# Optimization experiments

Hardware: AMD Instinct MI355X
Metric: run time of the kernel (lower is better)

Reference implementation:

```python
import jax, jax.numpy as jnp
import numpy as np

V = 256   # input_size / vocab
H = 1024  # hidden_size
B = 32
S = 512


def _uniform_w(key, shape, fan_in):
    k = float(np.sqrt(1.0 / fan_in))
    return jax.random.uniform(key, shape, minval=-k, maxval=k, dtype=jnp.float32)


def setup_inputs() -> dict:
    key = jax.random.key(0)
    ks = jax.random.split(key, 8)
    x = jax.random.randint(ks[0], (B, S), 0, V)
    # Gate order along last dim: [i, f, g, o] (concatenated per-gate weights,
    # mathematically identical to 8 separate small matmuls in the original).
    W_x0 = jnp.concatenate([_uniform_w(k, (V, H), V) for k in jax.random.split(ks[1], 4)], axis=1)
    W_h0 = jnp.concatenate([_uniform_w(k, (H, H), H) for k in jax.random.split(ks[2], 4)], axis=1)
    W_x1 = jnp.concatenate([_uniform_w(k, (H, H), H) for k in jax.random.split(ks[3], 4)], axis=1)
    W_h1 = jnp.concatenate([_uniform_w(k, (H, H), H) for k in jax.random.split(ks[4], 4)], axis=1)
    # biases: b_i=0, b_f=1, b_g=0, b_o=0
    b_gate = jnp.concatenate([jnp.zeros(H), jnp.ones(H), jnp.zeros(H), jnp.zeros(H)])
    b0 = b_gate
    b1 = b_gate
    W_hy = _uniform_w(ks[5], (H, V), H)
    b_y = jnp.zeros((V,), dtype=jnp.float32)
    return {"x": x, "W_x0": W_x0, "W_h0": W_h0, "b0": b0,
            "W_x1": W_x1, "W_h1": W_h1, "b1": b1,
            "W_hy": W_hy, "b_y": b_y}


def _cell(gates, c_prev):
    i, f, g, o = jnp.split(gates, 4, axis=-1)
    c = jax.nn.sigmoid(f) * c_prev + jax.nn.sigmoid(i) * jnp.tanh(g)
    h = jax.nn.sigmoid(o) * jnp.tanh(c)
    return h, c


def reference(x, W_x0, W_h0, b0, W_x1, W_h1, b1, W_hy, b_y):
    # x: (B, S) int -> one-hot (S, B, V)
    xe = jax.nn.one_hot(x, V, dtype=W_x0.dtype)          # (B, S, V)
    # precompute layer-0 input projection for all timesteps (same math)
    xproj = jnp.einsum('bsv,vg->sbg', xe, W_x0) + b0     # (S, B, 4H)

    def step(carry, xp_t):
        h0, c0, h1, c1 = carry
        h0n, c0n = _cell(xp_t + h0 @ W_h0, c0)
        h1n, c1n = _cell(h0n @ W_x1 + h1 @ W_h1 + b1, c1)
        out = h1n @ W_hy + b_y                           # (B, V)
        return (h0n, c0n, h1n, c1n), out

    z = jnp.zeros((x.shape[0], H), dtype=W_x0.dtype)
    _, outs = jax.lax.scan(step, (z, z, z, z), xproj)
    return outs                                          # (S, B, V)
```

## Files before the change

kernel.cpp:

```cpp
#include <hip/hip_runtime.h>
#include <math.h>


typedef __attribute__((ext_vector_type(8))) short short8;
typedef __attribute__((ext_vector_type(4))) float f32x4;

constexpr int kV = 256, kH = 1024, kB = 32, kS = 512, G4H = 4096;
constexpr int NT = 512, NBLK = 208;
constexpr int NA = 64, B0 = 64, C0 = 192, ROOT = NBLK - 1;

constexpr long SZW = 4194304L;
constexpr long SZY = 262144L;
constexpr long WP0H = 0,        WP0L = SZW;
constexpr long WP1XH = 2*SZW,   WP1XL = 3*SZW;
constexpr long WP1HH = 4*SZW,   WP1HL = 5*SZW;
constexpr long WYH  = 6*SZW,    WYL  = 6*SZW + SZY;
constexpr long HOFF = 6*SZW + 2*SZY;

#define MFMA(a,b,c) __builtin_amdgcn_mfma_f32_16x16x32_bf16(a, b, c, 0, 0, 0)

#define VM_WAIT(n) do { \
    asm volatile("s_waitcnt vmcnt(" #n ")" ::: "memory"); \
    __builtin_amdgcn_sched_barrier(0); \
  } while (0)

#define WLOAD(dst, p) \
  asm volatile("global_load_dwordx4 %0, %1, off" : "=v"(dst) : "v"(p) : "memory")

__device__ __forceinline__ float sigmoidf_(float v) { return 1.f / (1.f + expf(-v)); }

__device__ __forceinline__ void bf16split(float w, unsigned& hi, unsigned& lo) {
  unsigned u = __float_as_uint(w);
  unsigned r = (u + 0x7fffu + ((u >> 16) & 1u)) >> 16;
  float res = w - __uint_as_float(r << 16);
  unsigned u2 = __float_as_uint(res);
  unsigned r2 = (u2 + 0x7fffu + ((u2 >> 16) & 1u)) >> 16;
  hi = r; lo = r2;
}


__device__ __forceinline__ void coh_store_u32(unsigned* p, unsigned v) {
  asm volatile("global_store_dword %0, %1, off sc0 sc1" :: "v"(p), "v"(v) : "memory");
}
__device__ __forceinline__ void coh_store_u16(unsigned short* p, unsigned v) {
  asm volatile("global_store_short %0, %1, off sc0 sc1" :: "v"(p), "v"(v) : "memory");
}
__device__ __forceinline__ unsigned coh_load_u32(const unsigned* p) {
  unsigned v;
  asm volatile("global_load_dword %0, %1, off sc0 sc1\n\ts_waitcnt vmcnt(0)"
               : "=v"(v) : "v"(p) : "memory");
  return v;
}

__device__ __forceinline__ void stage_issue4(const unsigned short* pr0h,
                                             const unsigned short* pr1h,
                                             const unsigned short* pr0l,
                                             const unsigned short* pr1l,
                                             int qoff,
                                             float4& a, float4& b,
                                             float4& c, float4& d) {
  asm volatile(
      "global_load_dwordx4 %0, %4, off sc0 sc1\n\t"
      "global_load_dwordx4 %1, %5, off sc0 sc1\n\t"
      "global_load_dwordx4 %2, %6, off sc0 sc1\n\t"
      "global_load_dwordx4 %3, %7, off sc0 sc1"
      : "=&v"(a), "=&v"(b), "=&v"(c), "=&v"(d)
      : "v"(pr0h + qoff), "v"(pr1h + qoff), "v"(pr0l + qoff), "v"(pr1l + qoff)
      : "memory");
}

__device__ __forceinline__ void stage_write4(short8* HH, short8* HL,
                                             int b0_, int kg,
                                             const float4& a, const float4& b,
                                             const float4& c, const float4& d) {
  HH[b0_ * 33 + kg]        = __builtin_bit_cast(short8, a);
  HH[(b0_ + 16) * 33 + kg] = __builtin_bit_cast(short8, b);
  HL[b0_ * 33 + kg]        = __builtin_bit_cast(short8, c);
  HL[(b0_ + 16) * 33 + kg] = __builtin_bit_cast(short8, d);
}

__device__ __forceinline__ void lds_barrier() {
  asm volatile("s_waitcnt lgkmcnt(0)" ::: "memory");
  __builtin_amdgcn_sched_barrier(0);
  __builtin_amdgcn_s_barrier();
  __builtin_amdgcn_sched_barrier(0);
}


__device__ __forceinline__ void flag_barrier(unsigned* arrive, unsigned* gen,
                                             int blk, int tid, int t) {
  __syncthreads();
  const unsigned target = (unsigned)(t + 1);
  if (tid == 0) coh_store_u32(arrive + blk * 16, target);
  if (blk == ROOT) {
    if (tid < 64) {
      const unsigned* q0 = arrive + tid * 16;
      const unsigned* q1 = arrive + (64 + tid) * 16;
      const unsigned* q2 = arrive + (128 + tid) * 16;
      const int i3 = (192 + tid < NBLK) ? (192 + tid) : 0;
      const unsigned* q3 = arrive + i3 * 16;
      int guard = 0;
      for (;;) {
        unsigned a, b, c, d;
        asm volatile(
            "global_load_dword %0, %4, off sc0 sc1\n\t"
            "global_load_dword %1, %5, off sc0 sc1\n\t"
            "global_load_dword %2, %6, off sc0 sc1\n\t"
            "global_load_dword %3, %7, off sc0 sc1\n\t"
            "s_waitcnt vmcnt(0)"
            : "=&v"(a), "=&v"(b), "=&v"(c), "=&v"(d)
            : "v"(q0), "v"(q1), "v"(q2), "v"(q3) : "memory");
        bool ok = (a >= target) && (b >= target) && (c >= target) && (d >= target);
        if (__all(ok)) break;
        if (++guard > (1 << 17)) break;
      }
      if (tid == 0) coh_store_u32(gen, target);
    }
  } else {
    if (tid == 0) {
      int guard = 0;
      while (coh_load_u32(gen) < target) {
        __builtin_amdgcn_s_sleep(1);
        if (++guard > (1 << 17)) break;
      }
    }
  }
  __syncthreads();
}


__global__ void pack_w(const float* __restrict__ in, unsigned short* __restrict__ hi,
                       unsigned short* __restrict__ lo, int ncols) {
  int id = blockIdx.x * 256 + threadIdx.x;
  int slab = id / ncols, row = id % ncols;
  int k0 = (slab >> 2) * 32 + (slab & 3) * 8;
  long ob = ((long)slab * ncols + row) * 8;
  #pragma unroll
  for (int e = 0; e < 8; ++e) {
    float w = in[(long)(k0 + e) * ncols + row];
    unsigned h_, l_;
    bf16split(w, h_, l_);
    hi[ob + e] = (unsigned short)h_;
    lo[ob + e] = (unsigned short)l_;
  }
}

__global__ void zero_state(unsigned* __restrict__ p, int n) {
  int i = blockIdx.x * 256 + threadIdx.x;
  if (i < n) p[i] = 0u;
}


extern "C" __global__ void __launch_bounds__(512, 1)
lstm_persist(const int* __restrict__ x,
             const float* __restrict__ Wx0,
             const float* __restrict__ b0v,
             const float* __restrict__ b1v,
             const float* __restrict__ byv,
             unsigned short* __restrict__ wss,
             float* __restrict__ out) {
  const short8* wp0h  = (const short8*)(wss + WP0H);
  const short8* wp0l  = (const short8*)(wss + WP0L);
  const short8* wp1xh = (const short8*)(wss + WP1XH);
  const short8* wp1xl = (const short8*)(wss + WP1XL);
  const short8* wp1hh = (const short8*)(wss + WP1HH);
  const short8* wp1hl = (const short8*)(wss + WP1HL);
  const short8* wyh   = (const short8*)(wss + WYH);
  const short8* wyl   = (const short8*)(wss + WYL);
  unsigned short* h0h = wss + HOFF;
  unsigned short* h0l = h0h + 65536;
  unsigned short* h1h = h0h + 131072;
  unsigned short* h1l = h0h + 196608;
  unsigned* arrive = (unsigned*)(h0h + 262144);
  unsigned* gen = arrive + 4096;

  const int tid = threadIdx.x, blk = blockIdx.x;
  const int lane = tid & 63, m = lane & 15, quad = lane >> 4, w = tid >> 6;
  const int b0_ = tid >> 5, kg = tid & 31;
  const int kg8 = kg * 8;

  __shared__ short8 HSH[2][32 * 33];
  __shared__ short8 HSL[2][32 * 33];
  __shared__ float gx[4096];

  if (blk < NA) {
    const int g = w >> 1, kh = w & 1, j0A = blk * 16;
    const int ue = tid >> 5, be = tid & 31, j2e = j0A + ue;
    const float bA0 = b0v[j2e],          bA1 = b0v[kH + j2e];
    const float bA2 = b0v[2 * kH + j2e], bA3 = b0v[3 * kH + j2e];
    const short8* ah_ = wp0h + quad * 4096 + (g * 1024 + j0A + m);
    const short8* al_ = wp0l + quad * 4096 + (g * 1024 + j0A + m);
    short8 wah[16], wal[16];
    #pragma unroll
    for (int i = 0; i < 16; ++i) {
      WLOAD(wah[i], &ah_[(2 * i + kh) * 16384]);
      WLOAD(wal[i], &al_[(2 * i + kh) * 16384]);
    }
    VM_WAIT(0);
    float c0r = 0.f;

    #pragma unroll 1
    for (int t = 0; t < kS + 2; ++t) {
      const int s = t;
      if (s < kS) {
        const int rpar = (s + 1) & 1;
        const unsigned short* gH = h0h + rpar * 32768;
        const unsigned short* gL = h0l + rpar * 32768;
        const unsigned short* pH0 = gH + b0_ * 1024 + kg8;
        const unsigned short* pH1 = pH0 + 16 * 1024;
        const unsigned short* pL0 = gL + b0_ * 1024 + kg8;
        const unsigned short* pL1 = pL0 + 16 * 1024;
        const int xs = x[be * kS + s];
        const float* wxp = Wx0 + (long)xs * G4H + j2e;
        float wxi, wxf, wxg, wxo;
        asm volatile(
            "global_load_dword %0, %4, off\n\t"
            "global_load_dword %1, %5, off\n\t"
            "global_load_dword %2, %6, off\n\t"
            "global_load_dword %3, %7, off"
            : "=&v"(wxi), "=&v"(wxf), "=&v"(wxg), "=&v"(wxo)
            : "v"(wxp), "v"(wxp + kH), "v"(wxp + 2 * kH), "v"(wxp + 3 * kH)
            : "memory");
        float4 st[2][4];
        stage_issue4(pH0, pH1, pL0, pL1, 0, st[0][0], st[0][1], st[0][2], st[0][3]);
        f32x4 acc0 = {0.f, 0.f, 0.f, 0.f}, acc1 = {0.f, 0.f, 0.f, 0.f};
        #pragma unroll
        for (int ph = 0; ph < 4; ++ph) {
          if (ph < 3)
            stage_issue4(pH0, pH1, pL0, pL1, (ph + 1) * 256,
                         st[(ph + 1) & 1][0], st[(ph + 1) & 1][1],
                         st[(ph + 1) & 1][2], st[(ph + 1) & 1][3]);
          if (ph < 3) { VM_WAIT(4); } else { VM_WAIT(0); }
          stage_write4(&HSH[ph & 1][0], &HSL[ph & 1][0], b0_, kg,
                       st[ph & 1][0], st[ph & 1][1], st[ph & 1][2], st[ph & 1][3]);
          lds_barrier();
          #pragma unroll
          for (int i2 = 0; i2 < 4; ++i2) {
            const int kl = 2 * i2 + kh;
            const int widx = ph * 4 + i2;
            short8 bh0 = HSH[ph & 1][m * 33 + kl * 4 + quad];
            short8 bl0 = HSL[ph & 1][m * 33 + kl * 4 + quad];
            short8 bh1 = HSH[ph & 1][(16 + m) * 33 + kl * 4 + quad];
            short8 bl1 = HSL[ph & 1][(16 + m) * 33 + kl * 4 + quad];
            acc0 = MFMA(wah[widx], bh0, acc0);
            acc0 = MFMA(wah[widx], bl0, acc0);
            acc0 = MFMA(wal[widx], bh0, acc0);
            acc1 = MFMA(wah[widx], bh1, acc1);
            acc1 = MFMA(wah[widx], bl1, acc1);
            acc1 = MFMA(wal[widx], bh1, acc1);
          }
        }
        #pragma unroll
        for (int r = 0; r < 4; ++r) {
          gx[(kh * 64 + g * 16 + quad * 4 + r) * 32 + m]      = acc0[r];
          gx[(kh * 64 + g * 16 + quad * 4 + r) * 32 + 16 + m] = acc1[r];
        }
        lds_barrier();
        {
          float gi = gx[(0 + ue) * 32 + be]  + gx[(64 + 0 + ue) * 32 + be]  + wxi + bA0;
          float gf = gx[(16 + ue) * 32 + be] + gx[(64 + 16 + ue) * 32 + be] + wxf + bA1;
          float gg = gx[(32 + ue) * 32 + be] + gx[(64 + 32 + ue) * 32 + be] + wxg + bA2;
          float go = gx[(48 + ue) * 32 + be] + gx[(64 + 48 + ue) * 32 + be] + wxo + bA3;
          float cc = sigmoidf_(gf) * c0r + sigmoidf_(gi) * tanhf(gg);
          float hh = sigmoidf_(go) * tanhf(cc);
          c0r = cc;
          unsigned h_, l_;
          bf16split(hh, h_, l_);
          const int wpar = s & 1;
          coh_store_u16(h0h + wpar * 32768 + be * 1024 + j2e, h_);
          coh_store_u16(h0l + wpar * 32768 + be * 1024 + j2e, l_);
        }
      }
      if (t < kS + 1) flag_barrier(arrive, gen, blk, tid, t);
    }
  } else if (blk < C0) {
    const int hf = w >> 2, mt = (w >> 1) & 1, kq = w & 1;
    const int rowB = mt * 16 + m;
    const int growB = (rowB >> 3) * 1024 + (blk - B0) * 8 + (rowB & 7);
    const int ub = tid >> 5, bb2 = tid & 31;
    const int j2b = (blk - B0) * 8 + (ub & 7);
    const float bB0 = b1v[j2b],          bB1 = b1v[kH + j2b];
    const float bB2 = b1v[2 * kH + j2b], bB3 = b1v[3 * kH + j2b];
    const short8* bh_ = (hf ? wp1hh : wp1xh) + quad * 4096 + growB;
    const short8* bl_ = (hf ? wp1hl : wp1xl) + quad * 4096 + growB;
    short8 wbh[16], wbl[16];
    #pragma unroll
    for (int i = 0; i < 16; ++i) {
      WLOAD(wbh[i], &bh_[(2 * i + kq) * 16384]);
      WLOAD(wbl[i], &bl_[(2 * i + kq) * 16384]);
    }
    VM_WAIT(0);
    float c1r = 0.f;

    #pragma unroll 1
    for (int t = 0; t < kS + 2; ++t) {
      const int s = t - 1;
      if (s >= 0 && s < kS) {
        const unsigned short* g0h = h0h + (s & 1) * 32768;
        const unsigned short* g0l = h0l + (s & 1) * 32768;
        const unsigned short* g1h = h1h + ((s + 1) & 1) * 32768;
        const unsigned short* g1l = h1l + ((s + 1) & 1) * 32768;
        const unsigned short* pA0h = g0h + b0_ * 1024 + kg8;
        const unsigned short* pA1h = pA0h + 16 * 1024;
        const unsigned short* pA0l = g0l + b0_ * 1024 + kg8;
        const unsigned short* pA1l = pA0l + 16 * 1024;
        const unsigned short* pB0h = g1h + b0_ * 1024 + kg8;
        const unsigned short* pB1h = pB0h + 16 * 1024;
        const unsigned short* pB0l = g1l + b0_ * 1024 + kg8;
        const unsigned short* pB1l = pB0l + 16 * 1024;
        float4 st[2][4];
        stage_issue4(pA0h, pA1h, pA0l, pA1l, 0,
                     st[0][0], st[0][1], st[0][2], st[0][3]);
        f32x4 acc0 = {0.f, 0.f, 0.f, 0.f}, acc1 = {0.f, 0.f, 0.f, 0.f};
        #pragma unroll
        for (int ph = 0; ph < 8; ++ph) {
          const int half = ph >> 2, qtr = ph & 3;
          if (ph < 7) {
            const int p1 = ph + 1, q1 = p1 & 3;
            if ((p1 >> 2) == 0)
              stage_issue4(pA0h, pA1h, pA0l, pA1l, q1 * 256,
                           st[p1 & 1][0], st[p1 & 1][1], st[p1 & 1][2], st[p1 & 1][3]);
            else
              stage_issue4(pB0h, pB1h, pB0l, pB1l, q1 * 256,
                           st[p1 & 1][0], st[p1 & 1][1], st[p1 & 1][2], st[p1 & 1][3]);
          }
          if (ph < 7) { VM_WAIT(4); } else { VM_WAIT(0); }
          stage_write4(&HSH[ph & 1][0], &HSL[ph & 1][0], b0_, kg,
                       st[ph & 1][0], st[ph & 1][1], st[ph & 1][2], st[ph & 1][3]);
          lds_barrier();
          if (hf == half) {
            #pragma unroll
            for (int i2 = 0; i2 < 4; ++i2) {
              const int kl = 2 * i2 + kq;
              const int widx = qtr * 4 + i2;
              short8 bh0 = HSH[ph & 1][m * 33 + kl * 4 + quad];
              short8 bl0 = HSL[ph & 1][m * 33 + kl * 4 + quad];
              short8 bh1 = HSH[ph & 1][(16 + m) * 33 + kl * 4 + quad];
              short8 bl1 = HSL[ph & 1][(16 + m) * 33 + kl * 4 + quad];
              acc0 = MFMA(wbh[widx], bh0, acc0);
              acc0 = MFMA(wbh[widx], bl0, acc0);
              acc0 = MFMA(wbl[widx], bh0, acc0);
              acc1 = MFMA(wbh[widx], bh1, acc1);
              acc1 = MFMA(wbh[widx], bl1, acc1);
              acc1 = MFMA(wbl[widx], bh1, acc1);
            }
          }
        }
        #pragma unroll
        for (int r = 0; r < 4; ++r) {
          const int rg = hf * 2 + kq;
          gx[(rg * 32 + mt * 16 + quad * 4 + r) * 32 + m]      = acc0[r];
          gx[(rg * 32 + mt * 16 + quad * 4 + r) * 32 + 16 + m] = acc1[r];
        }
        lds_barrier();
        if (tid < 256) {
          const int u = tid >> 5, b = tid & 31;
          float gt[4];
          #pragma unroll
          for (int g2 = 0; g2 < 4; ++g2) {
            const int row = g2 * 8 + u;
            gt[g2] = gx[(row) * 32 + b] + gx[(32 + row) * 32 + b] +
                     gx[(64 + row) * 32 + b] + gx[(96 + row) * 32 + b];
          }
          float gt0 = gt[0] + bB0, gt1 = gt[1] + bB1;
          float gt2 = gt[2] + bB2, gt3 = gt[3] + bB3;
          float cc = sigmoidf_(gt1) * c1r + sigmoidf_(gt0) * tanhf(gt2);
          float hh = sigmoidf_(gt3) * tanhf(cc);
          c1r = cc;
          unsigned h_, l_;
          bf16split(hh, h_, l_);
          const int wpar = s & 1;
          const int j2 = (blk - B0) * 8 + u;
          coh_store_u16(h1h + wpar * 32768 + b * 1024 + j2, h_);
          coh_store_u16(h1l + wpar * 32768 + b * 1024 + j2, l_);
        }
        (void)ub; (void)bb2;
      }
      if (t < kS + 1) flag_barrier(arrive, gen, blk, tid, t);
    }
  } else {
    const int growC = (blk - C0) * 16 + m;
    const float byr = byv[(blk - C0) * 16 + (tid & 15)];
    const short8* ch_ = wyh + quad * 256 + growC;
    const short8* cl_ = wyl + quad * 256 + growC;
    short8 wch[4], wcl[4];
    #pragma unroll
    for (int i = 0; i < 4; ++i) {
      WLOAD(wch[i], &ch_[(i * 8 + w) * 1024]);
      WLOAD(wcl[i], &cl_[(i * 8 + w) * 1024]);
    }
    VM_WAIT(0);

    #pragma unroll 1
    for (int t = 0; t < kS + 2; ++t) {
      const int s = t - 2;
      if (s >= 0 && s < kS) {
        const int rpar = s & 1;
        const unsigned short* gH = h1h + rpar * 32768;
        const unsigned short* gL = h1l + rpar * 32768;
        const unsigned short* pH0 = gH + b0_ * 1024 + kg8;
        const unsigned short* pH1 = pH0 + 16 * 1024;
        const unsigned short* pL0 = gL + b0_ * 1024 + kg8;
        const unsigned short* pL1 = pL0 + 16 * 1024;
        float4 st[2][4];
        stage_issue4(pH0, pH1, pL0, pL1, 0, st[0][0], st[0][1], st[0][2], st[0][3]);
        f32x4 acc0 = {0.f, 0.f, 0.f, 0.f}, acc1 = {0.f, 0.f, 0.f, 0.f};
        #pragma unroll
        for (int ph = 0; ph < 4; ++ph) {
          if (ph < 3)
            stage_issue4(pH0, pH1, pL0, pL1, (ph + 1) * 256,
                         st[(ph + 1) & 1][0], st[(ph + 1) & 1][1],
                         st[(ph + 1) & 1][2], st[(ph + 1) & 1][3]);
          if (ph < 3) { VM_WAIT(4); } else { VM_WAIT(0); }
          stage_write4(&HSH[ph & 1][0], &HSL[ph & 1][0], b0_, kg,
                       st[ph & 1][0], st[ph & 1][1], st[ph & 1][2], st[ph & 1][3]);
          lds_barrier();
          {
            const int kl = w;
            short8 bh0 = HSH[ph & 1][m * 33 + kl * 4 + quad];
            short8 bl0 = HSL[ph & 1][m * 33 + kl * 4 + quad];
            short8 bh1 = HSH[ph & 1][(16 + m) * 33 + kl * 4 + quad];
            short8 bl1 = HSL[ph & 1][(16 + m) * 33 + kl * 4 + quad];
            acc0 = MFMA(wch[ph], bh0, acc0);
            acc0 = MFMA(wch[ph], bl0, acc0);
            acc0 = MFMA(wcl[ph], bh0, acc0);
            acc1 = MFMA(wch[ph], bh1, acc1);
            acc1 = MFMA(wch[ph], bl1, acc1);
            acc1 = MFMA(wcl[ph], bh1, acc1);
          }
        }
        #pragma unroll
        for (int r = 0; r < 4; ++r) {
          gx[(w * 16 + quad * 4 + r) * 32 + m]      = acc0[r];
          gx[(w * 16 + quad * 4 + r) * 32 + 16 + m] = acc1[r];
        }
        lds_barrier();
        {
          const int b = tid >> 4, vl = tid & 15;
          const int vg = (blk - C0) * 16 + vl;
          float sum = byr;
          #pragma unroll
          for (int rg = 0; rg < 8; ++rg) sum += gx[(rg * 16 + vl) * 32 + b];
          out[(s * kB + b) * kV + vg] = sum;
        }
      }
      if (t < kS + 1) flag_barrier(arrive, gen, blk, tid, t);
    }
  }
}


extern "C" void kernel_launch(void* const* d_in, const int* in_sizes, int n_in,
                              void* d_out, int out_size, void* d_ws, size_t ws_size,
                              hipStream_t stream) {
  const int*   x   = (const int*)d_in[0];
  const float* Wx0 = (const float*)d_in[1];
  const float* Wh0 = (const float*)d_in[2];
  const float* b0v = (const float*)d_in[3];
  const float* Wx1 = (const float*)d_in[4];
  const float* Wh1 = (const float*)d_in[5];
  const float* b1v = (const float*)d_in[6];
  const float* Why = (const float*)d_in[7];
  const float* byv = (const float*)d_in[8];
  unsigned short* wss = (unsigned short*)d_ws;
  float* outp = (float*)d_out;

  hipLaunchKernelGGL(pack_w, dim3(2048), dim3(256), 0, stream,
                     Wh0, wss + WP0H, wss + WP0L, G4H);
  hipLaunchKernelGGL(pack_w, dim3(2048), dim3(256), 0, stream,
                     Wx1, wss + WP1XH, wss + WP1XL, G4H);
  hipLaunchKernelGGL(pack_w, dim3(2048), dim3(256), 0, stream,
                     Wh1, wss + WP1HH, wss + WP1HL, G4H);
  hipLaunchKernelGGL(pack_w, dim3(128), dim3(256), 0, stream,
                     Why, wss + WYH, wss + WYL, kV);
  hipLaunchKernelGGL(zero_state, dim3(529), dim3(256), 0, stream,
                     (unsigned*)(wss + HOFF), 131072 + 4100);

  hipLaunchKernelGGL(lstm_persist, dim3(NBLK), dim3(NT), 0, stream,
                     x, Wx0, b0v, b1v, byv, wss, outp);
}
```

Measured before the change: 4.124 ms.

## Replace root-gated grid barrier with all-block polling and deepen hidden-state prefetch

The grid barrier no longer routes through a root block that gathers all arrivals and then publishes a generation word. Every block's first wavefront now polls all 208 arrival flags directly, which takes one cross-block hop out of each timestep's synchronization. In exchange, all blocks generate polling traffic on the flags. The hidden-state staging loads are also issued four phases deep up front instead of double-buffered one ahead, which uses more registers in return for more memory-level parallelism.

```diff
diff --git a/kernel.cpp b/kernel.cpp
--- a/kernel.cpp
+++ b/kernel.cpp
@@ -7,7 +7,7 @@
 
 constexpr int kV = 256, kH = 1024, kB = 32, kS = 512, G4H = 4096;
 constexpr int NT = 512, NBLK = 208;
-constexpr int NA = 64, B0 = 64, C0 = 192, ROOT = NBLK - 1;
+constexpr int NA = 64, B0 = 64, C0 = 192;
 
 constexpr long SZW = 4194304L;
 constexpr long SZY = 262144L;
@@ -44,12 +44,6 @@
 }
 __device__ __forceinline__ void coh_store_u16(unsigned short* p, unsigned v) {
   asm volatile("global_store_short %0, %1, off sc0 sc1" :: "v"(p), "v"(v) : "memory");
-}
-__device__ __forceinline__ unsigned coh_load_u32(const unsigned* p) {
-  unsigned v;
-  asm volatile("global_load_dword %0, %1, off sc0 sc1\n\ts_waitcnt vmcnt(0)"
-               : "=v"(v) : "v"(p) : "memory");
-  return v;
 }
 
 __device__ __forceinline__ void stage_issue4(const unsigned short* pr0h,
@@ -87,42 +81,32 @@
 }
 
 
-__device__ __forceinline__ void flag_barrier(unsigned* arrive, unsigned* gen,
+__device__ __forceinline__ void flag_barrier(unsigned* arrive,
                                              int blk, int tid, int t) {
   __syncthreads();
   const unsigned target = (unsigned)(t + 1);
   if (tid == 0) coh_store_u32(arrive + blk * 16, target);
-  if (blk == ROOT) {
-    if (tid < 64) {
-      const unsigned* q0 = arrive + tid * 16;
-      const unsigned* q1 = arrive + (64 + tid) * 16;
-      const unsigned* q2 = arrive + (128 + tid) * 16;
-      const int i3 = (192 + tid < NBLK) ? (192 + tid) : 0;
-      const unsigned* q3 = arrive + i3 * 16;
-      int guard = 0;
-      for (;;) {
-        unsigned a, b, c, d;
-        asm volatile(
-            "global_load_dword %0, %4, off sc0 sc1\n\t"
-            "global_load_dword %1, %5, off sc0 sc1\n\t"
-            "global_load_dword %2, %6, off sc0 sc1\n\t"
-            "global_load_dword %3, %7, off sc0 sc1\n\t"
-            "s_waitcnt vmcnt(0)"
-            : "=&v"(a), "=&v"(b), "=&v"(c), "=&v"(d)
-            : "v"(q0), "v"(q1), "v"(q2), "v"(q3) : "memory");
-        bool ok = (a >= target) && (b >= target) && (c >= target) && (d >= target);
-        if (__all(ok)) break;
-        if (++guard > (1 << 17)) break;
-      }
-      if (tid == 0) coh_store_u32(gen, target);
-    }
-  } else {
-    if (tid == 0) {
-      int guard = 0;
-      while (coh_load_u32(gen) < target) {
-        __builtin_amdgcn_s_sleep(1);
-        if (++guard > (1 << 17)) break;
-      }
+  if (tid < 64) {
+    const unsigned* q0 = arrive + tid * 16;
+    const unsigned* q1 = arrive + (64 + tid) * 16;
+    const unsigned* q2 = arrive + (128 + tid) * 16;
+    const int i3 = (192 + tid < NBLK) ? (192 + tid) : 0;
+    const unsigned* q3 = arrive + i3 * 16;
+    int guard = 0;
+    for (;;) {
+      unsigned a, b, c, d;
+      asm volatile(
+          "global_load_dword %0, %4, off sc0 sc1\n\t"
+          "global_load_dword %1, %5, off sc0 sc1\n\t"
+          "global_load_dword %2, %6, off sc0 sc1\n\t"
+          "global_load_dword %3, %7, off sc0 sc1\n\t"
+          "s_waitcnt vmcnt(0)"
+          : "=&v"(a), "=&v"(b), "=&v"(c), "=&v"(d)
+          : "v"(q0), "v"(q1), "v"(q2), "v"(q3) : "memory");
+      bool ok = (a >= target) && (b >= target) && (c >= target) && (d >= target);
+      if (__all(ok)) break;
+      __builtin_amdgcn_s_sleep(1);
+      if (++guard > (1 << 17)) break;
     }
   }
   __syncthreads();
@@ -172,7 +156,6 @@
   unsigned short* h1h = h0h + 131072;
   unsigned short* h1l = h0h + 196608;
   unsigned* arrive = (unsigned*)(h0h + 262144);
-  unsigned* gen = arrive + 4096;
 
   const int tid = threadIdx.x, blk = blockIdx.x;
   const int lane = tid & 63, m = lane & 15, quad = lane >> 4, w = tid >> 6;
@@ -221,18 +204,20 @@
             : "=&v"(wxi), "=&v"(wxf), "=&v"(wxg), "=&v"(wxo)
             : "v"(wxp), "v"(wxp + kH), "v"(wxp + 2 * kH), "v"(wxp + 3 * kH)
             : "memory");
-        float4 st[2][4];
-        stage_issue4(pH0, pH1, pL0, pL1, 0, st[0][0], st[0][1], st[0][2], st[0][3]);
+        float4 st[4][4];
+        stage_issue4(pH0, pH1, pL0, pL1, 0,   st[0][0], st[0][1], st[0][2], st[0][3]);
+        stage_issue4(pH0, pH1, pL0, pL1, 256, st[1][0], st[1][1], st[1][2], st[1][3]);
+        stage_issue4(pH0, pH1, pL0, pL1, 512, st[2][0], st[2][1], st[2][2], st[2][3]);
+        stage_issue4(pH0, pH1, pL0, pL1, 768, st[3][0], st[3][1], st[3][2], st[3][3]);
         f32x4 acc0 = {0.f, 0.f, 0.f, 0.f}, acc1 = {0.f, 0.f, 0.f, 0.f};
         #pragma unroll
         for (int ph = 0; ph < 4; ++ph) {
-          if (ph < 3)
-            stage_issue4(pH0, pH1, pL0, pL1, (ph + 1) * 256,
-                         st[(ph + 1) & 1][0], st[(ph + 1) & 1][1],
-                         st[(ph + 1) & 1][2], st[(ph + 1) & 1][3]);
-          if (ph < 3) { VM_WAIT(4); } else { VM_WAIT(0); }
+          if (ph == 0)      { VM_WAIT(12); }
+          else if (ph == 1) { VM_WAIT(8);  }
+          else if (ph == 2) { VM_WAIT(4);  }
+          else              { VM_WAIT(0);  }
           stage_write4(&HSH[ph & 1][0], &HSL[ph & 1][0], b0_, kg,
-                       st[ph & 1][0], st[ph & 1][1], st[ph & 1][2], st[ph & 1][3]);
+                       st[ph][0], st[ph][1], st[ph][2], st[ph][3]);
           lds_barrier();
           #pragma unroll
           for (int i2 = 0; i2 < 4; ++i2) {
@@ -271,13 +256,13 @@
           coh_store_u16(h0l + wpar * 32768 + be * 1024 + j2e, l_);
         }
       }
-      if (t < kS + 1) flag_barrier(arrive, gen, blk, tid, t);
+      if (t < kS + 1) flag_barrier(arrive, blk, tid, t);
     }
   } else if (blk < C0) {
     const int hf = w >> 2, mt = (w >> 1) & 1, kq = w & 1;
     const int rowB = mt * 16 + m;
     const int growB = (rowB >> 3) * 1024 + (blk - B0) * 8 + (rowB & 7);
-    const int ub = tid >> 5, bb2 = tid & 31;
+    const int ub = tid >> 5;
     const int j2b = (blk - B0) * 8 + (ub & 7);
     const float bB0 = b1v[j2b],          bB1 = b1v[kH + j2b];
     const float bB2 = b1v[2 * kH + j2b], bB3 = b1v[3 * kH + j2b];
@@ -308,26 +293,25 @@
         const unsigned short* pB1h = pB0h + 16 * 1024;
         const unsigned short* pB0l = g1l + b0_ * 1024 + kg8;
         const unsigned short* pB1l = pB0l + 16 * 1024;
-        float4 st[2][4];
-        stage_issue4(pA0h, pA1h, pA0l, pA1l, 0,
-                     st[0][0], st[0][1], st[0][2], st[0][3]);
+        float4 st[4][4];
+        stage_issue4(pA0h, pA1h, pA0l, pA1l, 0,   st[0][0], st[0][1], st[0][2], st[0][3]);
+        stage_issue4(pA0h, pA1h, pA0l, pA1l, 256, st[1][0], st[1][1], st[1][2], st[1][3]);
+        stage_issue4(pA0h, pA1h, pA0l, pA1l, 512, st[2][0], st[2][1], st[2][2], st[2][3]);
+        stage_issue4(pA0h, pA1h, pA0l, pA1l, 768, st[3][0], st[3][1], st[3][2], st[3][3]);
         f32x4 acc0 = {0.f, 0.f, 0.f, 0.f}, acc1 = {0.f, 0.f, 0.f, 0.f};
         #pragma unroll
         for (int ph = 0; ph < 8; ++ph) {
           const int half = ph >> 2, qtr = ph & 3;
-          if (ph < 7) {
-            const int p1 = ph + 1, q1 = p1 & 3;
-            if ((p1 >> 2) == 0)
-              stage_issue4(pA0h, pA1h, pA0l, pA1l, q1 * 256,
-                           st[p1 & 1][0], st[p1 & 1][1], st[p1 & 1][2], st[p1 & 1][3]);
-            else
-              stage_issue4(pB0h, pB1h, pB0l, pB1l, q1 * 256,
-                           st[p1 & 1][0], st[p1 & 1][1], st[p1 & 1][2], st[p1 & 1][3]);
-          }
-          if (ph < 7) { VM_WAIT(4); } else { VM_WAIT(0); }
+          if (ph < 5)       { VM_WAIT(12); }
+          else if (ph == 5) { VM_WAIT(8);  }
+          else if (ph == 6) { VM_WAIT(4);  }
+          else              { VM_WAIT(0);  }
           stage_write4(&HSH[ph & 1][0], &HSL[ph & 1][0], b0_, kg,
-                       st[ph & 1][0], st[ph & 1][1], st[ph & 1][2], st[ph & 1][3]);
+                       st[ph & 3][0], st[ph & 3][1], st[ph & 3][2], st[ph & 3][3]);
           lds_barrier();
+          if (ph < 4)
+            stage_issue4(pB0h, pB1h, pB0l, pB1l, ph * 256,
+                         st[ph & 3][0], st[ph & 3][1], st[ph & 3][2], st[ph & 3][3]);
           if (hf == half) {
             #pragma unroll
             for (int i2 = 0; i2 < 4; ++i2) {
@@ -374,9 +358,8 @@
           coh_store_u16(h1h + wpar * 32768 + b * 1024 + j2, h_);
           coh_store_u16(h1l + wpar * 32768 + b * 1024 + j2, l_);
         }
-        (void)ub; (void)bb2;
       }
-      if (t < kS + 1) flag_barrier(arrive, gen, blk, tid, t);
+      if (t < kS + 1) flag_barrier(arrive, blk, tid, t);
     }
   } else {
     const int growC = (blk - C0) * 16 + m;
@@ -402,18 +385,20 @@
         const unsigned short* pH1 = pH0 + 16 * 1024;
         const unsigned short* pL0 = gL + b0_ * 1024 + kg8;
         const unsigned short* pL1 = pL0 + 16 * 1024;
-        float4 st[2][4];
-        stage_issue4(pH0, pH1, pL0, pL1, 0, st[0][0], st[0][1], st[0][2], st[0][3]);
+        float4 st[4][4];
+        stage_issue4(pH0, pH1, pL0, pL1, 0,   st[0][0], st[0][1], st[0][2], st[0][3]);
+        stage_issue4(pH0, pH1, pL0, pL1, 256, st[1][0], st[1][1], st[1][2], st[1][3]);
+        stage_issue4(pH0, pH1, pL0, pL1, 512, st[2][0], st[2][1], st[2][2], st[2][3]);
+        stage_issue4(pH0, pH1, pL0, pL1, 768, st[3][0], st[3][1], st[3][2], st[3][3]);
         f32x4 acc0 = {0.f, 0.f, 0.f, 0.f}, acc1 = {0.f, 0.f, 0.f, 0.f};
         #pragma unroll
         for (int ph = 0; ph < 4; ++ph) {
-          if (ph < 3)
-            stage_issue4(pH0, pH1, pL0, pL1, (ph + 1) * 256,
-                         st[(ph + 1) & 1][0], st[(ph + 1) & 1][1],
-                         st[(ph + 1) & 1][2], st[(ph + 1) & 1][3]);
-          if (ph < 3) { VM_WAIT(4); } else { VM_WAIT(0); }
+          if (ph == 0)      { VM_WAIT(12); }
+          else if (ph == 1) { VM_WAIT(8);  }
+          else if (ph == 2) { VM_WAIT(4);  }
+          else              { VM_WAIT(0);  }
           stage_write4(&HSH[ph & 1][0], &HSL[ph & 1][0], b0_, kg,
-                       st[ph & 1][0], st[ph & 1][1], st[ph & 1][2], st[ph & 1][3]);
+                       st[ph][0], st[ph][1], st[ph][2], st[ph][3]);
           lds_barrier();
           {
             const int kl = w;
@@ -444,7 +429,7 @@
           out[(s * kB + b) * kV + vg] = sum;
         }
       }
-      if (t < kS + 1) flag_barrier(arrive, gen, blk, tid, t);
+      if (t < kS + 1) flag_barrier(arrive, blk, tid, t);
     }
   }
 }
```

Measured after the change: 4.619 ms. 1.12x slower.
